# Optimization experiments

Measured on AMD Instinct MI355X. Metric: run time of the kernel, lower is better.

## Reference

```python
import jax, jax.numpy as jnp
import numpy as np

B, S, H = 2, 2048, 2048
E, I, SH = 8, 768, 5632
TOP_K = 2


def setup_inputs() -> dict:
    key = jax.random.key(0)
    ks = jax.random.split(key, 8)
    sc = lambda *shape: 1.0 / np.sqrt(shape[-2] if len(shape) > 1 else 1.0)
    return {
        "hidden_states": jax.random.normal(ks[0], (B, S, H), jnp.float32),
        "router_w": jax.random.normal(ks[1], (H, E), jnp.float32) * (1.0 / np.sqrt(H)),
        "expert_gate_up_w": jax.random.normal(ks[2], (E, H, 2 * I), jnp.float32) * (1.0 / np.sqrt(H)),
        "expert_down_w": jax.random.normal(ks[3], (E, I, H), jnp.float32) * (1.0 / np.sqrt(I)),
        "shared_gate_w": jax.random.normal(ks[4], (H, SH), jnp.float32) * (1.0 / np.sqrt(H)),
        "shared_up_w": jax.random.normal(ks[5], (H, SH), jnp.float32) * (1.0 / np.sqrt(H)),
        "shared_down_w": jax.random.normal(ks[6], (SH, H), jnp.float32) * (1.0 / np.sqrt(SH)),
        "shared_expert_gate_w": jax.random.normal(ks[7], (H, 1), jnp.float32) * (1.0 / np.sqrt(H)),
    }


def reference(hidden_states, router_w, expert_gate_up_w, expert_down_w,
              shared_gate_w, shared_up_w, shared_down_w, shared_expert_gate_w):
    b, s, h = hidden_states.shape
    x = hidden_states.reshape(-1, h)  # [T, H]

    # Shared expert (SwiGLU) gated by sigmoid scalar gate per token.
    gate = jax.nn.silu((x @ shared_gate_w).astype(jnp.float32)).astype(x.dtype)
    shared_out = (gate * (x @ shared_up_w)) @ shared_down_w  # [T, H]
    shared_out = jax.nn.sigmoid(x @ shared_expert_gate_w) * shared_out

    # Router: softmax -> top-k -> renormalize -> dense routing weights [E, T].
    router_logits = x @ router_w  # [T, E]
    router_probs = jax.nn.softmax(router_logits, axis=-1)
    top_p, top_i = jax.lax.top_k(router_probs, TOP_K)  # [T, k]
    top_p = top_p / jnp.sum(top_p, axis=-1, keepdims=True)
    one_hot = jax.nn.one_hot(top_i, E, dtype=top_p.dtype)  # [T, k, E]
    routing_full = jnp.sum(one_hot * top_p[..., None], axis=1)  # [T, E]
    routing_full = routing_full.T.astype(x.dtype)  # [E, T]

    # Dense per-expert SwiGLU over all tokens (as in source einsums).
    gate_up = jnp.einsum('th,ehm->etm', x, expert_gate_up_w)  # [E, T, 2I]
    g, u = jnp.split(gate_up, 2, axis=-1)
    g = jax.nn.silu(g.astype(jnp.float32)).astype(x.dtype)
    expert_out = jnp.einsum('eti,eih->eth', u * g, expert_down_w)  # [E, T, H]

    expert_contribution = jnp.sum(expert_out * routing_full[:, :, None], axis=0)  # [T, H]
    out = (expert_contribution + shared_out).reshape(b, s, h)
    return out, router_logits
```

## Files before the change

kernel.cpp:

```cpp
#include <hip/hip_runtime.h>
#include <hip/hip_bf16.h>
#include <stdint.h>

#define DEVFN static __device__ __forceinline__

typedef __attribute__((ext_vector_type(8))) short bf16x8;
typedef __attribute__((ext_vector_type(4))) float f32x4;
typedef unsigned short u16;
typedef unsigned int u32;
typedef unsigned long long u64;

DEVFN u16 f2bf(float f) {
    union { float f; u32 u; } v; v.f = f;
    u32 r = v.u + 0x7FFFu + ((v.u >> 16) & 1u);
    return (u16)(r >> 16);
}

DEVFN void g2l16(const void* g, void* l) {
    __builtin_amdgcn_global_load_lds(
        (const __attribute__((address_space(1))) u32*)g,
        (__attribute__((address_space(3))) u32*)l, 16, 0, 0);
}

DEVFN void hbar() {
    __asm__ __volatile__("" ::: "memory");
    __builtin_amdgcn_s_barrier();
    __asm__ __volatile__("" ::: "memory");
}
DEVFN void vm4() { asm volatile("s_waitcnt vmcnt(4)" ::: "memory"); }
DEVFN void vm0() { asm volatile("s_waitcnt vmcnt(0)" ::: "memory"); }

#define MFMA16(a, b, c) __builtin_amdgcn_mfma_f32_16x16x32_bf16(a, b, c, 0, 0, 0)

__global__ __launch_bounds__(512, 2) void gemm8_swiglu_k(
    const u16* __restrict__ A, const u16* __restrict__ Bg,
    const u16* __restrict__ Bu, u16* __restrict__ out,
    int K, int nx, int ldc)
{
    extern __shared__ char smraw[];
    char* smA = smraw;
    char* smB = smraw + 65536;

    const int tid = threadIdx.x;
    const int lane = tid & 63, wv = tid >> 6;
    const int wm = wv >> 2, wn = wv & 3;
    const int l15 = lane & 15, kg = lane >> 4;

    const int nwg = gridDim.x;
    const int id = (blockIdx.x & 7) * (nwg >> 3) + (blockIdx.x >> 3);
    const int m0 = (id / nx) * 256, n0 = (id % nx) * 128;

    const u16* Ap  = A  + (long)m0 * K;
    const u16* Bgp = Bg + (long)n0 * K;
    const u16* Bup = Bu + (long)n0 * K;

    f32x4 accg[8][2], accu[8][2];
#pragma unroll
    for (int i = 0; i < 8; ++i)
#pragma unroll
        for (int j = 0; j < 2; ++j) {
            accg[i][j] = f32x4{0.f, 0.f, 0.f, 0.f};
            accu[i][j] = f32x4{0.f, 0.f, 0.f, 0.f};
        }

    auto stA = [&](int kt, int hh, int buf) {
        const u16* src = Ap + ((long)hh * 128) * K + kt * 64;
        char* dst = smA + buf * 32768 + hh * 16384;
#pragma unroll
        for (int i = 0; i < 2; ++i) {
            int slot = i * 512 + tid;
            int row = slot >> 3, ch = slot & 7;
            g2l16(src + (long)row * K + ((ch ^ (row & 7)) << 3), dst + slot * 16);
        }
    };
    auto stB = [&](int kt, int hh, int buf) {
        const u16* src = (hh ? Bup : Bgp) + kt * 64;
        char* dst = smB + buf * 32768 + hh * 16384;
#pragma unroll
        for (int i = 0; i < 2; ++i) {
            int slot = i * 512 + tid;
            int row = slot >> 3, ch = slot & 7;
            g2l16(src + (long)row * K + ((ch ^ (row & 7)) << 3), dst + slot * 16);
        }
    };
    auto frag = [&](const char* base, int r, int c) -> bf16x8 {
        return *(const __attribute__((address_space(3))) bf16x8*)
            (base + r * 128 + (((c) ^ (r & 7)) << 4));
    };

    stA(0, 0, 0); stA(0, 1, 0);
    stB(0, 0, 0); stB(0, 1, 0);
    stB(1, 0, 1); stB(1, 1, 1);
    vm4();
    hbar();

    const int nk = K >> 6;
    for (int kt = 0; kt < nk; kt += 2) {
        const bool more = (kt + 2) < nk;
#pragma unroll
        for (int h = 0; h < 2; ++h) {
            const char* ab = smA + h * 32768;
            const char* bb = smB + h * 32768;
            bf16x8 bgv[2][2], buv[2][2];
#pragma unroll
            for (int p = 0; p < 4; ++p) {
                if (p == 0) {
#pragma unroll
                    for (int fn = 0; fn < 2; ++fn)
#pragma unroll
                        for (int s = 0; s < 2; ++s) {
                            int rB = wn * 32 + fn * 16 + l15;
                            bgv[fn][s] = frag(bb, rB, s * 4 + kg);
                            buv[fn][s] = frag(bb + 16384, rB, s * 4 + kg);
                        }
                }
                bf16x8 av[2][2];
#pragma unroll
                for (int am = 0; am < 2; ++am)
#pragma unroll
                    for (int s = 0; s < 2; ++s)
                        av[am][s] = frag(ab, wm * 128 + (p * 2 + am) * 16 + l15,
                                         s * 4 + kg);
                if (h == 0) {
                    if (p == 1)      { stA(kt + 1, 0, 1); stA(kt + 1, 1, 1); }
                    else if (p == 2) { if (more) stB(kt + 2, 0, 0); }
                    else if (p == 3) {
                        if (more) { stB(kt + 2, 1, 0); vm4(); } else vm0();
                    }
                } else {
                    if (more) {
                        if (p == 1)      stA(kt + 2, 0, 0);
                        else if (p == 2) { stA(kt + 2, 1, 0); stB(kt + 3, 0, 1); }
                        else if (p == 3) { stB(kt + 3, 1, 1); vm4(); }
                    }
                }
                hbar();
                __builtin_amdgcn_sched_barrier(0);
                __builtin_amdgcn_s_setprio(1);
#pragma unroll
                for (int am = 0; am < 2; ++am)
#pragma unroll
                    for (int s = 0; s < 2; ++s)
#pragma unroll
                        for (int fn = 0; fn < 2; ++fn) {
                            accg[p * 2 + am][fn] = MFMA16(av[am][s], bgv[fn][s],
                                                          accg[p * 2 + am][fn]);
                            accu[p * 2 + am][fn] = MFMA16(av[am][s], buv[fn][s],
                                                          accu[p * 2 + am][fn]);
                        }
                __builtin_amdgcn_s_setprio(0);
            }
        }
    }

    const int lq = lane >> 4;
#pragma unroll
    for (int fm = 0; fm < 8; ++fm)
#pragma unroll
        for (int j = 0; j < 4; ++j) {
            int row = m0 + wm * 128 + fm * 16 + lq * 4 + j;
#pragma unroll
            for (int fn = 0; fn < 2; ++fn) {
                int col = n0 + wn * 32 + fn * 16 + l15;
                float g = accg[fm][fn][j], u = accu[fm][fn][j];
                float s = g * (1.f / (1.f + __expf(-g))) * u;
                out[(long)row * ldc + col] = f2bf(s);
            }
        }
}

__global__ __launch_bounds__(512, 2) void gemm8e_swiglu_k(
    const u16* __restrict__ xb, const u16* __restrict__ Beg,
    const u16* __restrict__ Beu, const int* __restrict__ tok,
    const int* __restrict__ cntp, u16* __restrict__ eact,
    int K, int ldc, int cap)
{
    const int e = blockIdx.z;
    const int m0 = blockIdx.y * 256;
    if (m0 >= cntp[e]) return;
    const int n0 = blockIdx.x * 128;

    extern __shared__ char smraw[];
    char* smA = smraw;
    char* smB = smraw + 65536;

    const int tid = threadIdx.x;
    const int lane = tid & 63, wv = tid >> 6;
    const int wm = wv >> 2, wn = wv & 3;
    const int l15 = lane & 15, kg = lane >> 4;

    const int r0 = tid >> 3, ch = tid & 7;
    const int swz = (ch ^ (r0 & 7)) << 3;
    const int* tseg = tok + (long)e * cap + m0;
    const u16* pa00 = xb + (long)tseg[r0] * K + swz;
    const u16* pa01 = xb + (long)tseg[64 + r0] * K + swz;
    const u16* pa10 = xb + (long)tseg[128 + r0] * K + swz;
    const u16* pa11 = xb + (long)tseg[192 + r0] * K + swz;

    const u16* Bgp = Beg + ((long)e * ldc + n0) * K;
    const u16* Bup = Beu + ((long)e * ldc + n0) * K;

    f32x4 accg[8][2], accu[8][2];
#pragma unroll
    for (int i = 0; i < 8; ++i)
#pragma unroll
        for (int j = 0; j < 2; ++j) {
            accg[i][j] = f32x4{0.f, 0.f, 0.f, 0.f};
            accu[i][j] = f32x4{0.f, 0.f, 0.f, 0.f};
        }

    auto stA = [&](int kt, int hh, int buf) {
        char* dst = smA + buf * 32768 + hh * 16384;
        const u16* p0 = hh ? pa10 : pa00;
        const u16* p1 = hh ? pa11 : pa01;
        g2l16(p0 + kt * 64, dst + (long)tid * 16);
        g2l16(p1 + kt * 64, dst + (long)(512 + tid) * 16);
    };
    auto stB = [&](int kt, int hh, int buf) {
        const u16* src = (hh ? Bup : Bgp) + kt * 64;
        char* dst = smB + buf * 32768 + hh * 16384;
#pragma unroll
        for (int i = 0; i < 2; ++i) {
            int slot = i * 512 + tid;
            int row = slot >> 3, c = slot & 7;
            g2l16(src + (long)row * K + ((c ^ (row & 7)) << 3), dst + slot * 16);
        }
    };
    auto frag = [&](const char* base, int r, int c) -> bf16x8 {
        return *(const __attribute__((address_space(3))) bf16x8*)
            (base + r * 128 + (((c) ^ (r & 7)) << 4));
    };

    stA(0, 0, 0); stA(0, 1, 0);
    stB(0, 0, 0); stB(0, 1, 0);
    stB(1, 0, 1); stB(1, 1, 1);
    vm4();
    hbar();

    const int nk = K >> 6;
    for (int kt = 0; kt < nk; kt += 2) {
        const bool more = (kt + 2) < nk;
#pragma unroll
        for (int h = 0; h < 2; ++h) {
            const char* ab = smA + h * 32768;
            const char* bb = smB + h * 32768;
            bf16x8 bgv[2][2], buv[2][2];
#pragma unroll
            for (int p = 0; p < 4; ++p) {
                if (p == 0) {
#pragma unroll
                    for (int fn = 0; fn < 2; ++fn)
#pragma unroll
                        for (int s = 0; s < 2; ++s) {
                            int rB = wn * 32 + fn * 16 + l15;
                            bgv[fn][s] = frag(bb, rB, s * 4 + kg);
                            buv[fn][s] = frag(bb + 16384, rB, s * 4 + kg);
                        }
                }
                bf16x8 av[2][2];
#pragma unroll
                for (int am = 0; am < 2; ++am)
#pragma unroll
                    for (int s = 0; s < 2; ++s)
                        av[am][s] = frag(ab, wm * 128 + (p * 2 + am) * 16 + l15,
                                         s * 4 + kg);
                if (h == 0) {
                    if (p == 0)      { stA(kt + 1, 0, 1); stA(kt + 1, 1, 1); }
                    else if (p == 1) { if (more) stB(kt + 2, 0, 0); }
                    else if (p == 2) { if (more) stB(kt + 2, 1, 0); }
                    else             { if (more) vm4(); else vm0(); }
                } else {
                    if (more) {
                        if (p == 0)      stA(kt + 2, 0, 0);
                        else if (p == 1) stA(kt + 2, 1, 0);
                        else if (p == 2) stB(kt + 3, 0, 1);
                        else             { stB(kt + 3, 1, 1); vm4(); }
                    }
                }
                hbar();
                __builtin_amdgcn_sched_barrier(0);
                __builtin_amdgcn_s_setprio(1);
#pragma unroll
                for (int am = 0; am < 2; ++am)
#pragma unroll
                    for (int s = 0; s < 2; ++s)
#pragma unroll
                        for (int fn = 0; fn < 2; ++fn) {
                            accg[p * 2 + am][fn] = MFMA16(av[am][s], bgv[fn][s],
                                                          accg[p * 2 + am][fn]);
                            accu[p * 2 + am][fn] = MFMA16(av[am][s], buv[fn][s],
                                                          accu[p * 2 + am][fn]);
                        }
                __builtin_amdgcn_s_setprio(0);
                __builtin_amdgcn_sched_barrier(0);
                hbar();
            }
        }
    }

    const int lq = lane >> 4;
#pragma unroll
    for (int fm = 0; fm < 8; ++fm)
#pragma unroll
        for (int j = 0; j < 4; ++j) {
            long row = (long)e * cap + m0 + wm * 128 + fm * 16 + lq * 4 + j;
#pragma unroll
            for (int fn = 0; fn < 2; ++fn) {
                int col = n0 + wn * 32 + fn * 16 + l15;
                float g = accg[fm][fn][j], u = accu[fm][fn][j];
                float s = g * (1.f / (1.f + __expf(-g))) * u;
                eact[row * ldc + col] = f2bf(s);
            }
        }
}

template<int NSLOT>
DEVFN void stage(const u16* __restrict__ src, int ldk, u16* lds, int tid) {
#pragma unroll
    for (int i = 0; i < NSLOT / 256; ++i) {
        int slot = i * 256 + tid;
        int row = slot >> 2, chunk = slot & 3;
        int kg = chunk ^ ((row >> 1) & 3);
        g2l16(src + (long)row * ldk + kg * 8, lds + slot * 8);
    }
}

DEVFN bf16x8 ld_frag(const u16* lds, int row, int kg) {
    int chunk = kg ^ ((row >> 1) & 3);
    const u16* p = lds + row * 32 + chunk * 8;
    return *(const __attribute__((address_space(3))) bf16x8*)p;
}

__global__ __launch_bounds__(256) void gemm_down_k(
    const u16* __restrict__ A, const u16* __restrict__ B,
    float* __restrict__ C, const float* __restrict__ gvec,
    int K, int ldc)
{
    __shared__ u16 sm[2][8192];
    const int tid = threadIdx.x;
    const int lane = tid & 63, wv = tid >> 6;
    const int wm = wv >> 1, wn = wv & 1;
    const int m0 = blockIdx.y * 128, n0 = blockIdx.x * 128;
    const u16* Ab = A + (long)m0 * K;
    const u16* Bb = B + (long)n0 * K;

    f32x4 acc[4][4];
#pragma unroll
    for (int i = 0; i < 4; ++i)
#pragma unroll
        for (int j = 0; j < 4; ++j) acc[i][j] = f32x4{0.f, 0.f, 0.f, 0.f};

    stage<512>(Ab, K, &sm[0][0], tid);
    stage<512>(Bb, K, &sm[0][4096], tid);

    const int nk = K >> 5;
    for (int kt = 0; kt < nk; ++kt) {
        const int cur = kt & 1;
        __syncthreads();
        if (kt + 1 < nk) {
            stage<512>(Ab + (kt + 1) * 32, K, &sm[cur ^ 1][0], tid);
            stage<512>(Bb + (kt + 1) * 32, K, &sm[cur ^ 1][4096], tid);
        }
        const int l15 = lane & 15, kg = lane >> 4;
        bf16x8 av[4], bv[4];
#pragma unroll
        for (int f = 0; f < 4; ++f) {
            av[f] = ld_frag(&sm[cur][0],    wm * 64 + f * 16 + l15, kg);
            bv[f] = ld_frag(&sm[cur][4096], wn * 64 + f * 16 + l15, kg);
        }
#pragma unroll
        for (int fm = 0; fm < 4; ++fm)
#pragma unroll
            for (int fn = 0; fn < 4; ++fn)
                acc[fm][fn] = MFMA16(av[fm], bv[fn], acc[fm][fn]);
    }

    const int l15 = lane & 15, lq = lane >> 4;
#pragma unroll
    for (int fm = 0; fm < 4; ++fm) {
#pragma unroll
        for (int j = 0; j < 4; ++j) {
            int row = m0 + wm * 64 + fm * 16 + lq * 4 + j;
            float gmul = gvec[row];
#pragma unroll
            for (int fn = 0; fn < 4; ++fn) {
                int col = n0 + wn * 64 + fn * 16 + l15;
                C[(long)row * ldc + col] = acc[fm][fn][j] * gmul;
            }
        }
    }
}

__global__ __launch_bounds__(256) void gemm_down_moe_k(
    const u16* __restrict__ eact, const u16* __restrict__ Bed,
    float* __restrict__ out, const int* __restrict__ tok,
    const float* __restrict__ wrow, const int* __restrict__ cntp,
    int K, int ldc, int cap)
{
    const int e = blockIdx.z;
    const int m0 = blockIdx.y * 128;
    if (m0 >= cntp[e]) return;
    const int n0 = blockIdx.x * 128;

    __shared__ u16 sm[2][8192];
    const int tid = threadIdx.x;
    const int lane = tid & 63, wv = tid >> 6;
    const int wm = wv >> 1, wn = wv & 1;
    const u16* Ab = eact + ((long)e * cap + m0) * K;
    const u16* Bb = Bed + (long)e * ldc * K + (long)n0 * K;

    f32x4 acc[4][4];
#pragma unroll
    for (int i = 0; i < 4; ++i)
#pragma unroll
        for (int j = 0; j < 4; ++j) acc[i][j] = f32x4{0.f, 0.f, 0.f, 0.f};

    stage<512>(Ab, K, &sm[0][0], tid);
    stage<512>(Bb, K, &sm[0][4096], tid);

    const int nk = K >> 5;
    for (int kt = 0; kt < nk; ++kt) {
        const int cur = kt & 1;
        __syncthreads();
        if (kt + 1 < nk) {
            stage<512>(Ab + (kt + 1) * 32, K, &sm[cur ^ 1][0], tid);
            stage<512>(Bb + (kt + 1) * 32, K, &sm[cur ^ 1][4096], tid);
        }
        const int l15 = lane & 15, kg = lane >> 4;
        bf16x8 av[4], bv[4];
#pragma unroll
        for (int f = 0; f < 4; ++f) {
            av[f] = ld_frag(&sm[cur][0],    wm * 64 + f * 16 + l15, kg);
            bv[f] = ld_frag(&sm[cur][4096], wn * 64 + f * 16 + l15, kg);
        }
#pragma unroll
        for (int fm = 0; fm < 4; ++fm)
#pragma unroll
            for (int fn = 0; fn < 4; ++fn)
                acc[fm][fn] = MFMA16(av[fm], bv[fn], acc[fm][fn]);
    }

    const int l15 = lane & 15, lq = lane >> 4;
#pragma unroll
    for (int fm = 0; fm < 4; ++fm) {
#pragma unroll
        for (int j = 0; j < 4; ++j) {
            long crow = (long)e * cap + m0 + wm * 64 + fm * 16 + lq * 4 + j;
            float w = wrow[crow];
            if (w != 0.f) {
                long t = tok[crow];
#pragma unroll
                for (int fn = 0; fn < 4; ++fn) {
                    int col = n0 + wn * 64 + fn * 16 + l15;
                    atomicAdd(out + t * ldc + col, acc[fm][fn][j] * w);
                }
            }
        }
    }
}

__global__ __launch_bounds__(256) void router_k(
    const float* __restrict__ x, const float* __restrict__ rw,
    const float* __restrict__ sgw, float* __restrict__ logits,
    int2* __restrict__ te, float2* __restrict__ tw,
    float* __restrict__ sig, int T, int H)
{
    const int tid = threadIdx.x, lane = tid & 63, wv = tid >> 6;
    const int t = blockIdx.x * 4 + wv;
    const float* xr = x + (long)t * H;
    float acc[8] = {0, 0, 0, 0, 0, 0, 0, 0};
    float as = 0.f;
    for (int h = lane; h < H; h += 64) {
        float xv = xr[h];
        const float* r = rw + h * 8;
#pragma unroll
        for (int e = 0; e < 8; ++e) acc[e] += xv * r[e];
        as += xv * sgw[h];
    }
#pragma unroll
    for (int off = 32; off; off >>= 1) {
#pragma unroll
        for (int e = 0; e < 8; ++e) acc[e] += __shfl_xor(acc[e], off);
        as += __shfl_xor(as, off);
    }
    if (lane == 0) {
        float mx = acc[0];
#pragma unroll
        for (int e = 1; e < 8; ++e) mx = fmaxf(mx, acc[e]);
        float p[8], sum = 0.f;
#pragma unroll
        for (int e = 0; e < 8; ++e) { p[e] = expf(acc[e] - mx); sum += p[e]; }
        int i1 = 0;
#pragma unroll
        for (int e = 1; e < 8; ++e) if (p[e] > p[i1]) i1 = e;
        int i2 = (i1 == 0) ? 1 : 0;
#pragma unroll
        for (int e = 0; e < 8; ++e) if (e != i1 && p[e] > p[i2]) i2 = e;
        float den = p[i1] + p[i2];
        te[t] = make_int2(i1, i2);
        tw[t] = make_float2(p[i1] / den, p[i2] / den);
#pragma unroll
        for (int e = 0; e < 8; ++e) logits[(long)t * 8 + e] = acc[e];
        sig[t] = 1.f / (1.f + expf(-as));
    }
}

__global__ __launch_bounds__(256) void compact_k(
    const int2* __restrict__ te, const float2* __restrict__ tw,
    int* __restrict__ tok, float* __restrict__ wrow,
    int* __restrict__ cntp, int T, int cap)
{
    const int e = blockIdx.x;
    const int tid = threadIdx.x, lane = tid & 63, wv = tid >> 6;
    __shared__ int wtot[4];
    int cnt = 0;
    for (int c0 = 0; c0 < T; c0 += 256) {
        int t = c0 + tid;
        int2 ids = te[t];
        float2 ws = tw[t];
        float w = (ids.x == e) ? ws.x : ((ids.y == e) ? ws.y : -1.f);
        bool sel = (w >= 0.f);
        u64 b = __ballot(sel);
        int rln = __popcll(b & ((1ull << lane) - 1ull));
        if (lane == 0) wtot[wv] = __popcll(b);
        __syncthreads();
        int rank = rln, tot = 0;
#pragma unroll
        for (int k = 0; k < 4; ++k) { if (k < wv) rank += wtot[k]; tot += wtot[k]; }
        if (sel) {
            int pos = cnt + rank;
            if (pos < cap) {
                tok[(long)e * cap + pos] = t;
                wrow[(long)e * cap + pos] = w;
            }
        }
        cnt += tot;
        __syncthreads();
    }
    if (cnt > cap) cnt = cap;
    int cp = (cnt + 255) & ~255;
    if (cp > cap) cp = cap;
    for (int p = cnt + tid; p < cp; p += 256) {
        tok[(long)e * cap + p] = 0;
        wrow[(long)e * cap + p] = 0.f;
    }
    if (tid == 0) cntp[e] = cp;
}

__global__ __launch_bounds__(256) void transpose_k(
    const float* __restrict__ src0, long src_zstr, int src_ld,
    u16* __restrict__ dst0, long dst_zstr, int dst_ld)
{
    __shared__ float tile[64][65];
    const float* src = src0 + (long)blockIdx.z * src_zstr;
    u16* dst = dst0 + (long)blockIdx.z * dst_zstr;
    int r0 = blockIdx.y * 64, c0 = blockIdx.x * 64;
    int tx = threadIdx.x & 63, ty = threadIdx.x >> 6;
#pragma unroll
    for (int k = 0; k < 16; ++k)
        tile[ty + 4 * k][tx] = src[(long)(r0 + ty + 4 * k) * src_ld + c0 + tx];
    __syncthreads();
#pragma unroll
    for (int k = 0; k < 16; ++k)
        dst[(long)(c0 + ty + 4 * k) * dst_ld + r0 + tx] = f2bf(tile[tx][ty + 4 * k]);
}

__global__ __launch_bounds__(256) void cvt_x_k(const float* __restrict__ x,
                                               u16* __restrict__ xb)
{
    long i = ((long)blockIdx.x * 256 + threadIdx.x) * 4;
    float4 v = *(const float4*)(x + i);
    union { u16 s[4]; uint2 v2; } o;
    o.s[0] = f2bf(v.x); o.s[1] = f2bf(v.y); o.s[2] = f2bf(v.z); o.s[3] = f2bf(v.w);
    *(uint2*)(xb + i) = o.v2;
}

extern "C" void kernel_launch(void* const* d_in, const int* in_sizes, int n_in,
                              void* d_out, int out_size, void* d_ws, size_t ws_size,
                              hipStream_t stream) {
    (void)in_sizes; (void)n_in; (void)out_size; (void)ws_size;
    const int Hd = 2048, E = 8, I = 768, SH = 5632, T = 4096, CAP = 2048;

    const float* x    = (const float*)d_in[0];
    const float* rw   = (const float*)d_in[1];
    const float* egu  = (const float*)d_in[2];
    const float* edw  = (const float*)d_in[3];
    const float* sgw  = (const float*)d_in[4];
    const float* suw  = (const float*)d_in[5];
    const float* sdw  = (const float*)d_in[6];
    const float* segw = (const float*)d_in[7];
    float* out = (float*)d_out;
    float* logits = out + (size_t)T * Hd;

    char* wsp = (char*)d_ws;
    size_t off = 0;
    auto alloc = [&](size_t bytes) {
        void* p = wsp + off; off += (bytes + 255) & ~(size_t)255; return p;
    };
    u16* xb   = (u16*)alloc((size_t)T * Hd * 2);
    u16* Bgs  = (u16*)alloc((size_t)SH * Hd * 2);
    u16* Bus  = (u16*)alloc((size_t)SH * Hd * 2);
    u16* Bds  = (u16*)alloc((size_t)Hd * SH * 2);
    u16* Beg  = (u16*)alloc((size_t)E * I * Hd * 2);
    u16* Beu  = (u16*)alloc((size_t)E * I * Hd * 2);
    u16* Bed  = (u16*)alloc((size_t)E * Hd * I * 2);
    u16* hs   = (u16*)alloc((size_t)T * SH * 2);
    u16* eact = (u16*)alloc((size_t)E * CAP * I * 2);
    int2*   te   = (int2*)alloc((size_t)T * 8);
    float2* tw   = (float2*)alloc((size_t)T * 8);
    int*    tok  = (int*)alloc((size_t)E * CAP * 4);
    float*  wrow = (float*)alloc((size_t)E * CAP * 4);
    int*    cntp = (int*)alloc(64);
    float*  sig  = (float*)alloc((size_t)T * 4);

    hipFuncSetAttribute((const void*)gemm8_swiglu_k,
                        hipFuncAttributeMaxDynamicSharedMemorySize, 131072);
    hipFuncSetAttribute((const void*)gemm8e_swiglu_k,
                        hipFuncAttributeMaxDynamicSharedMemorySize, 131072);

    cvt_x_k<<<(T * Hd) / 1024, 256, 0, stream>>>(x, xb);
    router_k<<<T / 4, 256, 0, stream>>>(x, rw, segw, logits, te, tw, sig, T, Hd);
    compact_k<<<E, 256, 0, stream>>>(te, tw, tok, wrow, cntp, T, CAP);

    transpose_k<<<dim3(SH / 64, Hd / 64), 256, 0, stream>>>(sgw, 0, SH, Bgs, 0, Hd);
    transpose_k<<<dim3(SH / 64, Hd / 64), 256, 0, stream>>>(suw, 0, SH, Bus, 0, Hd);
    transpose_k<<<dim3(Hd / 64, SH / 64), 256, 0, stream>>>(sdw, 0, Hd, Bds, 0, SH);
    transpose_k<<<dim3(I / 64, Hd / 64, E), 256, 0, stream>>>(
        egu, (long)Hd * 2 * I, 2 * I, Beg, (long)I * Hd, Hd);
    transpose_k<<<dim3(I / 64, Hd / 64, E), 256, 0, stream>>>(
        egu + I, (long)Hd * 2 * I, 2 * I, Beu, (long)I * Hd, Hd);
    transpose_k<<<dim3(Hd / 64, I / 64, E), 256, 0, stream>>>(
        edw, (long)I * Hd, Hd, Bed, (long)Hd * I, I);

    gemm8_swiglu_k<<<dim3((SH / 128) * (T / 256)), 512, 131072, stream>>>(
        xb, Bgs, Bus, hs, Hd, SH / 128, SH);
    gemm_down_k<<<dim3(Hd / 128, T / 128), 256, 0, stream>>>(
        hs, Bds, out, sig, SH, Hd);
    gemm8e_swiglu_k<<<dim3(I / 128, CAP / 256, E), 512, 131072, stream>>>(
        xb, Beg, Beu, tok, cntp, eact, Hd, I, CAP);
    gemm_down_moe_k<<<dim3(Hd / 128, CAP / 128, E), 256, 0, stream>>>(
        eact, Bed, out, tok, wrow, cntp, I, Hd, CAP);
}
```

Before: 581.3 us.

## Fuse shared and routed expert GEMMs into single grouped launches

Merges the shared-expert and routed-expert gate/up SwiGLU GEMMs into one kernel launch with a block-index split, and likewise merges both down-projection GEMMs into one launch. Shared-expert down output now accumulates via atomicAdd into a zeroed output buffer, allowing both paths to run concurrently and fill the GPU better. This removes launch gaps and tail underutilization, at the cost of extra atomics and a memset on the shared path.

After: 582.7 us. Within noise of the previous version (+0.2%).

```diff
diff --git a/kernel.cpp b/kernel.cpp
--- a/kernel.cpp
+++ b/kernel.cpp
@@ -32,10 +32,14 @@
 
 #define MFMA16(a, b, c) __builtin_amdgcn_mfma_f32_16x16x32_bf16(a, b, c, 0, 0, 0)
 
-__global__ __launch_bounds__(512, 2) void gemm8_swiglu_k(
-    const u16* __restrict__ A, const u16* __restrict__ Bg,
-    const u16* __restrict__ Bu, u16* __restrict__ out,
-    int K, int nx, int ldc)
+__global__ __launch_bounds__(512, 2) void gemm8_top_k(
+    const u16* __restrict__ xb,
+    const u16* __restrict__ Bgs, const u16* __restrict__ Bus,
+    u16* __restrict__ hs,
+    const u16* __restrict__ Beg, const u16* __restrict__ Beu,
+    const int* __restrict__ tok, const int* __restrict__ cntp,
+    u16* __restrict__ eact,
+    int K, int nwsw, int nxsw, int ldsw, int Ie, int cap)
 {
     extern __shared__ char smraw[];
     char* smA = smraw;
@@ -45,273 +49,260 @@
     const int lane = tid & 63, wv = tid >> 6;
     const int wm = wv >> 2, wn = wv & 3;
     const int l15 = lane & 15, kg = lane >> 4;
-
-    const int nwg = gridDim.x;
-    const int id = (blockIdx.x & 7) * (nwg >> 3) + (blockIdx.x >> 3);
-    const int m0 = (id / nx) * 256, n0 = (id % nx) * 128;
-
-    const u16* Ap  = A  + (long)m0 * K;
-    const u16* Bgp = Bg + (long)n0 * K;
-    const u16* Bup = Bu + (long)n0 * K;
-
-    f32x4 accg[8][2], accu[8][2];
-#pragma unroll
-    for (int i = 0; i < 8; ++i)
-#pragma unroll
-        for (int j = 0; j < 2; ++j) {
-            accg[i][j] = f32x4{0.f, 0.f, 0.f, 0.f};
-            accu[i][j] = f32x4{0.f, 0.f, 0.f, 0.f};
-        }
-
-    auto stA = [&](int kt, int hh, int buf) {
-        const u16* src = Ap + ((long)hh * 128) * K + kt * 64;
-        char* dst = smA + buf * 32768 + hh * 16384;
-#pragma unroll
-        for (int i = 0; i < 2; ++i) {
-            int slot = i * 512 + tid;
-            int row = slot >> 3, ch = slot & 7;
-            g2l16(src + (long)row * K + ((ch ^ (row & 7)) << 3), dst + slot * 16);
-        }
-    };
-    auto stB = [&](int kt, int hh, int buf) {
-        const u16* src = (hh ? Bup : Bgp) + kt * 64;
-        char* dst = smB + buf * 32768 + hh * 16384;
-#pragma unroll
-        for (int i = 0; i < 2; ++i) {
-            int slot = i * 512 + tid;
-            int row = slot >> 3, ch = slot & 7;
-            g2l16(src + (long)row * K + ((ch ^ (row & 7)) << 3), dst + slot * 16);
-        }
-    };
+    const int lq = lane >> 4;
+
     auto frag = [&](const char* base, int r, int c) -> bf16x8 {
         return *(const __attribute__((address_space(3))) bf16x8*)
             (base + r * 128 + (((c) ^ (r & 7)) << 4));
     };
 
-    stA(0, 0, 0); stA(0, 1, 0);
-    stB(0, 0, 0); stB(0, 1, 0);
-    stB(1, 0, 1); stB(1, 1, 1);
-    vm4();
-    hbar();
-
-    const int nk = K >> 6;
-    for (int kt = 0; kt < nk; kt += 2) {
-        const bool more = (kt + 2) < nk;
-#pragma unroll
-        for (int h = 0; h < 2; ++h) {
-            const char* ab = smA + h * 32768;
-            const char* bb = smB + h * 32768;
-            bf16x8 bgv[2][2], buv[2][2];
-#pragma unroll
-            for (int p = 0; p < 4; ++p) {
-                if (p == 0) {
-#pragma unroll
-                    for (int fn = 0; fn < 2; ++fn)
-#pragma unroll
-                        for (int s = 0; s < 2; ++s) {
-                            int rB = wn * 32 + fn * 16 + l15;
-                            bgv[fn][s] = frag(bb, rB, s * 4 + kg);
-                            buv[fn][s] = frag(bb + 16384, rB, s * 4 + kg);
+    if ((int)blockIdx.x < nwsw) {
+        const int id = (blockIdx.x & 7) * (nwsw >> 3) + (blockIdx.x >> 3);
+        const int m0 = (id / nxsw) * 256, n0 = (id % nxsw) * 128;
+
+        const u16* Ap  = xb  + (long)m0 * K;
+        const u16* Bgp = Bgs + (long)n0 * K;
+        const u16* Bup = Bus + (long)n0 * K;
+
+        f32x4 accg[8][2], accu[8][2];
+#pragma unroll
+        for (int i = 0; i < 8; ++i)
+#pragma unroll
+            for (int j = 0; j < 2; ++j) {
+                accg[i][j] = f32x4{0.f, 0.f, 0.f, 0.f};
+                accu[i][j] = f32x4{0.f, 0.f, 0.f, 0.f};
+            }
+
+        auto stA = [&](int kt, int hh, int buf) {
+            const u16* src = Ap + ((long)hh * 128) * K + kt * 64;
+            char* dst = smA + buf * 32768 + hh * 16384;
+#pragma unroll
+            for (int i = 0; i < 2; ++i) {
+                int slot = i * 512 + tid;
+                int row = slot >> 3, ch = slot & 7;
+                g2l16(src + (long)row * K + ((ch ^ (row & 7)) << 3),
+                      dst + slot * 16);
+            }
+        };
+        auto stB = [&](int kt, int hh, int buf) {
+            const u16* src = (hh ? Bup : Bgp) + kt * 64;
+            char* dst = smB + buf * 32768 + hh * 16384;
+#pragma unroll
+            for (int i = 0; i < 2; ++i) {
+                int slot = i * 512 + tid;
+                int row = slot >> 3, ch = slot & 7;
+                g2l16(src + (long)row * K + ((ch ^ (row & 7)) << 3),
+                      dst + slot * 16);
+            }
+        };
+
+        stA(0, 0, 0); stA(0, 1, 0);
+        stB(0, 0, 0); stB(0, 1, 0);
+        stB(1, 0, 1); stB(1, 1, 1);
+        vm4();
+        hbar();
+
+        const int nk = K >> 6;
+        for (int kt = 0; kt < nk; kt += 2) {
+            const bool more = (kt + 2) < nk;
+#pragma unroll
+            for (int h = 0; h < 2; ++h) {
+                const char* ab = smA + h * 32768;
+                const char* bb = smB + h * 32768;
+                bf16x8 bgv[2][2], buv[2][2];
+#pragma unroll
+                for (int p = 0; p < 4; ++p) {
+                    if (p == 0) {
+#pragma unroll
+                        for (int fn = 0; fn < 2; ++fn)
+#pragma unroll
+                            for (int s = 0; s < 2; ++s) {
+                                int rB = wn * 32 + fn * 16 + l15;
+                                bgv[fn][s] = frag(bb, rB, s * 4 + kg);
+                                buv[fn][s] = frag(bb + 16384, rB, s * 4 + kg);
+                            }
+                    }
+                    bf16x8 av[2][2];
+#pragma unroll
+                    for (int am = 0; am < 2; ++am)
+#pragma unroll
+                        for (int s = 0; s < 2; ++s)
+                            av[am][s] = frag(ab,
+                                wm * 128 + (p * 2 + am) * 16 + l15, s * 4 + kg);
+                    if (h == 0) {
+                        if (p == 1)      { stA(kt + 1, 0, 1); stA(kt + 1, 1, 1); }
+                        else if (p == 2) { if (more) stB(kt + 2, 0, 0); }
+                        else if (p == 3) {
+                            if (more) { stB(kt + 2, 1, 0); vm4(); } else vm0();
                         }
+                    } else {
+                        if (more) {
+                            if (p == 1)      stA(kt + 2, 0, 0);
+                            else if (p == 2) { stA(kt + 2, 1, 0);
+                                               stB(kt + 3, 0, 1); }
+                            else if (p == 3) { stB(kt + 3, 1, 1); vm4(); }
+                        }
+                    }
+                    hbar();
+                    __builtin_amdgcn_sched_barrier(0);
+                    __builtin_amdgcn_s_setprio(1);
+#pragma unroll
+                    for (int am = 0; am < 2; ++am)
+#pragma unroll
+                        for (int s = 0; s < 2; ++s)
+#pragma unroll
+                            for (int fn = 0; fn < 2; ++fn) {
+                                accg[p * 2 + am][fn] = MFMA16(av[am][s],
+                                    bgv[fn][s], accg[p * 2 + am][fn]);
+                                accu[p * 2 + am][fn] = MFMA16(av[am][s],
+                                    buv[fn][s], accu[p * 2 + am][fn]);
+                            }
+                    __builtin_amdgcn_s_setprio(0);
                 }
-                bf16x8 av[2][2];
-#pragma unroll
-                for (int am = 0; am < 2; ++am)
-#pragma unroll
-                    for (int s = 0; s < 2; ++s)
-                        av[am][s] = frag(ab, wm * 128 + (p * 2 + am) * 16 + l15,
-                                         s * 4 + kg);
-                if (h == 0) {
-                    if (p == 1)      { stA(kt + 1, 0, 1); stA(kt + 1, 1, 1); }
-                    else if (p == 2) { if (more) stB(kt + 2, 0, 0); }
-                    else if (p == 3) {
-                        if (more) { stB(kt + 2, 1, 0); vm4(); } else vm0();
+            }
+        }
+
+#pragma unroll
+        for (int fm = 0; fm < 8; ++fm)
+#pragma unroll
+            for (int j = 0; j < 4; ++j) {
+                int row = m0 + wm * 128 + fm * 16 + lq * 4 + j;
+#pragma unroll
+                for (int fn = 0; fn < 2; ++fn) {
+                    int col = n0 + wn * 32 + fn * 16 + l15;
+                    float g = accg[fm][fn][j], u = accu[fm][fn][j];
+                    float s = g * (1.f / (1.f + __expf(-g))) * u;
+                    hs[(long)row * ldsw + col] = f2bf(s);
+                }
+            }
+    } else {
+        const int bx = blockIdx.x - nwsw;
+        const int e = bx / 48;
+        const int rem = bx % 48;
+        const int m0 = (rem / 6) * 256;
+        if (m0 >= cntp[e]) return;
+        const int n0 = (rem % 6) * 128;
+
+        const int r0 = tid >> 3, ch = tid & 7;
+        const int swz = (ch ^ (r0 & 7)) << 3;
+        const int* tseg = tok + (long)e * cap + m0;
+        const u16* pa00 = xb + (long)tseg[r0] * K + swz;
+        const u16* pa01 = xb + (long)tseg[64 + r0] * K + swz;
+        const u16* pa10 = xb + (long)tseg[128 + r0] * K + swz;
+        const u16* pa11 = xb + (long)tseg[192 + r0] * K + swz;
+
+        const u16* Bgp = Beg + ((long)e * Ie + n0) * K;
+        const u16* Bup = Beu + ((long)e * Ie + n0) * K;
+
+        f32x4 accg[8][2], accu[8][2];
+#pragma unroll
+        for (int i = 0; i < 8; ++i)
+#pragma unroll
+            for (int j = 0; j < 2; ++j) {
+                accg[i][j] = f32x4{0.f, 0.f, 0.f, 0.f};
+                accu[i][j] = f32x4{0.f, 0.f, 0.f, 0.f};
+            }
+
+        auto stA = [&](int kt, int hh, int buf) {
+            char* dst = smA + buf * 32768 + hh * 16384;
+            const u16* p0 = hh ? pa10 : pa00;
+            const u16* p1 = hh ? pa11 : pa01;
+            g2l16(p0 + kt * 64, dst + (long)tid * 16);
+            g2l16(p1 + kt * 64, dst + (long)(512 + tid) * 16);
+        };
+        auto stB = [&](int kt, int hh, int buf) {
+            const u16* src = (hh ? Bup : Bgp) + kt * 64;
+            char* dst = smB + buf * 32768 + hh * 16384;
+#pragma unroll
+            for (int i = 0; i < 2; ++i) {
+                int slot = i * 512 + tid;
+                int row = slot >> 3, c = slot & 7;
+                g2l16(src + (long)row * K + ((c ^ (row & 7)) << 3),
+                      dst + slot * 16);
+            }
+        };
+
+        stA(0, 0, 0); stA(0, 1, 0);
+        stB(0, 0, 0); stB(0, 1, 0);
+        stB(1, 0, 1); stB(1, 1, 1);
+        vm4();
+        hbar();
+
+        const int nk = K >> 6;
+        for (int kt = 0; kt < nk; kt += 2) {
+            const bool more = (kt + 2) < nk;
+#pragma unroll
+            for (int h = 0; h < 2; ++h) {
+                const char* ab = smA + h * 32768;
+                const char* bb = smB + h * 32768;
+                bf16x8 bgv[2][2], buv[2][2];
+#pragma unroll
+                for (int p = 0; p < 4; ++p) {
+                    if (p == 0) {
+#pragma unroll
+                        for (int fn = 0; fn < 2; ++fn)
+#pragma unroll
+                            for (int s = 0; s < 2; ++s) {
+                                int rB = wn * 32 + fn * 16 + l15;
+                                bgv[fn][s] = frag(bb, rB, s * 4 + kg);
+                                buv[fn][s] = frag(bb + 16384, rB, s * 4 + kg);
+                            }
                     }
-                } else {
-                    if (more) {
-                        if (p == 1)      stA(kt + 2, 0, 0);
-                        else if (p == 2) { stA(kt + 2, 1, 0); stB(kt + 3, 0, 1); }
-                        else if (p == 3) { stB(kt + 3, 1, 1); vm4(); }
+                    bf16x8 av[2][2];
+#pragma unroll
+                    for (int am = 0; am < 2; ++am)
+#pragma unroll
+                        for (int s = 0; s < 2; ++s)
+                            av[am][s] = frag(ab,
+                                wm * 128 + (p * 2 + am) * 16 + l15, s * 4 + kg);
+                    if (h == 0) {
+                        if (p == 0)      { stA(kt + 1, 0, 1); stA(kt + 1, 1, 1); }
+                        else if (p == 1) { if (more) stB(kt + 2, 0, 0); }
+                        else if (p == 2) { if (more) stB(kt + 2, 1, 0); }
+                        else             { if (more) vm4(); else vm0(); }
+                    } else {
+                        if (more) {
+                            if (p == 0)      stA(kt + 2, 0, 0);
+                            else if (p == 1) stA(kt + 2, 1, 0);
+                            else if (p == 2) stB(kt + 3, 0, 1);
+                            else             { stB(kt + 3, 1, 1); vm4(); }
+                        }
                     }
+                    hbar();
+                    __builtin_amdgcn_sched_barrier(0);
+                    __builtin_amdgcn_s_setprio(1);
+#pragma unroll
+                    for (int am = 0; am < 2; ++am)
+#pragma unroll
+                        for (int s = 0; s < 2; ++s)
+#pragma unroll
+                            for (int fn = 0; fn < 2; ++fn) {
+                                accg[p * 2 + am][fn] = MFMA16(av[am][s],
+                                    bgv[fn][s], accg[p * 2 + am][fn]);
+                                accu[p * 2 + am][fn] = MFMA16(av[am][s],
+                                    buv[fn][s], accu[p * 2 + am][fn]);
+                            }
+                    __builtin_amdgcn_s_setprio(0);
+                    __builtin_amdgcn_sched_barrier(0);
+                    hbar();
                 }
-                hbar();
-                __builtin_amdgcn_sched_barrier(0);
-                __builtin_amdgcn_s_setprio(1);
-#pragma unroll
-                for (int am = 0; am < 2; ++am)
-#pragma unroll
-                    for (int s = 0; s < 2; ++s)
-#pragma unroll
-                        for (int fn = 0; fn < 2; ++fn) {
-                            accg[p * 2 + am][fn] = MFMA16(av[am][s], bgv[fn][s],
-                                                          accg[p * 2 + am][fn]);
-                            accu[p * 2 + am][fn] = MFMA16(av[am][s], buv[fn][s],
-                                                          accu[p * 2 + am][fn]);
-                        }
-                __builtin_amdgcn_s_setprio(0);
             }
         }
-    }
-
-    const int lq = lane >> 4;
-#pragma unroll
-    for (int fm = 0; fm < 8; ++fm)
-#pragma unroll
-        for (int j = 0; j < 4; ++j) {
-            int row = m0 + wm * 128 + fm * 16 + lq * 4 + j;
-#pragma unroll
-            for (int fn = 0; fn < 2; ++fn) {
-                int col = n0 + wn * 32 + fn * 16 + l15;
-                float g = accg[fm][fn][j], u = accu[fm][fn][j];
-                float s = g * (1.f / (1.f + __expf(-g))) * u;
-                out[(long)row * ldc + col] = f2bf(s);
-            }
-        }
-}
-
-__global__ __launch_bounds__(512, 2) void gemm8e_swiglu_k(
-    const u16* __restrict__ xb, const u16* __restrict__ Beg,
-    const u16* __restrict__ Beu, const int* __restrict__ tok,
-    const int* __restrict__ cntp, u16* __restrict__ eact,
-    int K, int ldc, int cap)
-{
-    const int e = blockIdx.z;
-    const int m0 = blockIdx.y * 256;
-    if (m0 >= cntp[e]) return;
-    const int n0 = blockIdx.x * 128;
-
-    extern __shared__ char smraw[];
-    char* smA = smraw;
-    char* smB = smraw + 65536;
-
-    const int tid = threadIdx.x;
-    const int lane = tid & 63, wv = tid >> 6;
-    const int wm = wv >> 2, wn = wv & 3;
-    const int l15 = lane & 15, kg = lane >> 4;
-
-    const int r0 = tid >> 3, ch = tid & 7;
-    const int swz = (ch ^ (r0 & 7)) << 3;
-    const int* tseg = tok + (long)e * cap + m0;
-    const u16* pa00 = xb + (long)tseg[r0] * K + swz;
-    const u16* pa01 = xb + (long)tseg[64 + r0] * K + swz;
-    const u16* pa10 = xb + (long)tseg[128 + r0] * K + swz;
-    const u16* pa11 = xb + (long)tseg[192 + r0] * K + swz;
-
-    const u16* Bgp = Beg + ((long)e * ldc + n0) * K;
-    const u16* Bup = Beu + ((long)e * ldc + n0) * K;
-
-    f32x4 accg[8][2], accu[8][2];
-#pragma unroll
-    for (int i = 0; i < 8; ++i)
-#pragma unroll
-        for (int j = 0; j < 2; ++j) {
-            accg[i][j] = f32x4{0.f, 0.f, 0.f, 0.f};
-            accu[i][j] = f32x4{0.f, 0.f, 0.f, 0.f};
-        }
-
-    auto stA = [&](int kt, int hh, int buf) {
-        char* dst = smA + buf * 32768 + hh * 16384;
-        const u16* p0 = hh ? pa10 : pa00;
-        const u16* p1 = hh ? pa11 : pa01;
-        g2l16(p0 + kt * 64, dst + (long)tid * 16);
-        g2l16(p1 + kt * 64, dst + (long)(512 + tid) * 16);
-    };
-    auto stB = [&](int kt, int hh, int buf) {
-        const u16* src = (hh ? Bup : Bgp) + kt * 64;
-        char* dst = smB + buf * 32768 + hh * 16384;
-#pragma unroll
-        for (int i = 0; i < 2; ++i) {
-            int slot = i * 512 + tid;
-            int row = slot >> 3, c = slot & 7;
-            g2l16(src + (long)row * K + ((c ^ (row & 7)) << 3), dst + slot * 16);
-        }
-    };
-    auto frag = [&](const char* base, int r, int c) -> bf16x8 {
-        return *(const __attribute__((address_space(3))) bf16x8*)
-            (base + r * 128 + (((c) ^ (r & 7)) << 4));
-    };
-
-    stA(0, 0, 0); stA(0, 1, 0);
-    stB(0, 0, 0); stB(0, 1, 0);
-    stB(1, 0, 1); stB(1, 1, 1);
-    vm4();
-    hbar();
-
-    const int nk = K >> 6;
-    for (int kt = 0; kt < nk; kt += 2) {
-        const bool more = (kt + 2) < nk;
-#pragma unroll
-        for (int h = 0; h < 2; ++h) {
-            const char* ab = smA + h * 32768;
-            const char* bb = smB + h * 32768;
-            bf16x8 bgv[2][2], buv[2][2];
-#pragma unroll
-            for (int p = 0; p < 4; ++p) {
-                if (p == 0) {
-#pragma unroll
-                    for (int fn = 0; fn < 2; ++fn)
-#pragma unroll
-                        for (int s = 0; s < 2; ++s) {
-                            int rB = wn * 32 + fn * 16 + l15;
-                            bgv[fn][s] = frag(bb, rB, s * 4 + kg);
-                            buv[fn][s] = frag(bb + 16384, rB, s * 4 + kg);
-                        }
+
+#pragma unroll
+        for (int fm = 0; fm < 8; ++fm)
+#pragma unroll
+            for (int j = 0; j < 4; ++j) {
+                long row = (long)e * cap + m0 + wm * 128 + fm * 16 + lq * 4 + j;
+#pragma unroll
+                for (int fn = 0; fn < 2; ++fn) {
+                    int col = n0 + wn * 32 + fn * 16 + l15;
+                    float g = accg[fm][fn][j], u = accu[fm][fn][j];
+                    float s = g * (1.f / (1.f + __expf(-g))) * u;
+                    eact[row * Ie + col] = f2bf(s);
                 }
-                bf16x8 av[2][2];
-#pragma unroll
-                for (int am = 0; am < 2; ++am)
-#pragma unroll
-                    for (int s = 0; s < 2; ++s)
-                        av[am][s] = frag(ab, wm * 128 + (p * 2 + am) * 16 + l15,
-                                         s * 4 + kg);
-                if (h == 0) {
-                    if (p == 0)      { stA(kt + 1, 0, 1); stA(kt + 1, 1, 1); }
-                    else if (p == 1) { if (more) stB(kt + 2, 0, 0); }
-                    else if (p == 2) { if (more) stB(kt + 2, 1, 0); }
-                    else             { if (more) vm4(); else vm0(); }
-                } else {
-                    if (more) {
-                        if (p == 0)      stA(kt + 2, 0, 0);
-                        else if (p == 1) stA(kt + 2, 1, 0);
-                        else if (p == 2) stB(kt + 3, 0, 1);
-                        else             { stB(kt + 3, 1, 1); vm4(); }
-                    }
-                }
-                hbar();
-                __builtin_amdgcn_sched_barrier(0);
-                __builtin_amdgcn_s_setprio(1);
-#pragma unroll
-                for (int am = 0; am < 2; ++am)
-#pragma unroll
-                    for (int s = 0; s < 2; ++s)
-#pragma unroll
-                        for (int fn = 0; fn < 2; ++fn) {
-                            accg[p * 2 + am][fn] = MFMA16(av[am][s], bgv[fn][s],
-                                                          accg[p * 2 + am][fn]);
-                            accu[p * 2 + am][fn] = MFMA16(av[am][s], buv[fn][s],
-                                                          accu[p * 2 + am][fn]);
-                        }
-                __builtin_amdgcn_s_setprio(0);
-                __builtin_amdgcn_sched_barrier(0);
-                hbar();
-            }
-        }
-    }
-
-    const int lq = lane >> 4;
-#pragma unroll
-    for (int fm = 0; fm < 8; ++fm)
-#pragma unroll
-        for (int j = 0; j < 4; ++j) {
-            long row = (long)e * cap + m0 + wm * 128 + fm * 16 + lq * 4 + j;
-#pragma unroll
-            for (int fn = 0; fn < 2; ++fn) {
-                int col = n0 + wn * 32 + fn * 16 + l15;
-                float g = accg[fm][fn][j], u = accu[fm][fn][j];
-                float s = g * (1.f / (1.f + __expf(-g))) * u;
-                eact[row * ldc + col] = f2bf(s);
-            }
-        }
+            }
+    }
 }
 
 template<int NSLOT>
@@ -331,18 +322,43 @@
     return *(const __attribute__((address_space(3))) bf16x8*)p;
 }
 
-__global__ __launch_bounds__(256) void gemm_down_k(
-    const u16* __restrict__ A, const u16* __restrict__ B,
-    float* __restrict__ C, const float* __restrict__ gvec,
-    int K, int ldc)
+__global__ __launch_bounds__(256) void gemm_down_fused_k(
+    const u16* __restrict__ hs, const u16* __restrict__ Bds,
+    const float* __restrict__ sig,
+    const u16* __restrict__ eact, const u16* __restrict__ Bed,
+    const int* __restrict__ tok, const float* __restrict__ wrow,
+    const int* __restrict__ cntp,
+    float* __restrict__ out,
+    int Ksh, int Ke, int ldc, int cap, int nwsd)
 {
     __shared__ u16 sm[2][8192];
     const int tid = threadIdx.x;
     const int lane = tid & 63, wv = tid >> 6;
     const int wm = wv >> 1, wn = wv & 1;
-    const int m0 = blockIdx.y * 128, n0 = blockIdx.x * 128;
-    const u16* Ab = A + (long)m0 * K;
-    const u16* Bb = B + (long)n0 * K;
+    const int l15 = lane & 15, kg = lane >> 4, lq = lane >> 4;
+
+    const u16 *Ab, *Bb;
+    int K;
+    int m0, n0;
+    int e = 0;
+    bool shared_path = ((int)blockIdx.x < nwsd);
+    if (shared_path) {
+        m0 = (blockIdx.x / 16) * 128;
+        n0 = (blockIdx.x % 16) * 128;
+        K = Ksh;
+        Ab = hs + (long)m0 * K;
+        Bb = Bds + (long)n0 * K;
+    } else {
+        int bx = blockIdx.x - nwsd;
+        e = bx >> 8;
+        int rem = bx & 255;
+        m0 = (rem >> 4) * 128;
+        if (m0 >= cntp[e]) return;
+        n0 = (rem & 15) * 128;
+        K = Ke;
+        Ab = eact + ((long)e * cap + m0) * K;
+        Bb = Bed + ((long)e * ldc + n0) * K;
+    }
 
     f32x4 acc[4][4];
 #pragma unroll
@@ -361,7 +377,6 @@
             stage<512>(Ab + (kt + 1) * 32, K, &sm[cur ^ 1][0], tid);
             stage<512>(Bb + (kt + 1) * 32, K, &sm[cur ^ 1][4096], tid);
         }
-        const int l15 = lane & 15, kg = lane >> 4;
         bf16x8 av[4], bv[4];
 #pragma unroll
         for (int f = 0; f < 4; ++f) {
@@ -375,87 +390,36 @@
                 acc[fm][fn] = MFMA16(av[fm], bv[fn], acc[fm][fn]);
     }
 
-    const int l15 = lane & 15, lq = lane >> 4;
-#pragma unroll
-    for (int fm = 0; fm < 4; ++fm) {
-#pragma unroll
-        for (int j = 0; j < 4; ++j) {
-            int row = m0 + wm * 64 + fm * 16 + lq * 4 + j;
-            float gmul = gvec[row];
-#pragma unroll
-            for (int fn = 0; fn < 4; ++fn) {
-                int col = n0 + wn * 64 + fn * 16 + l15;
-                C[(long)row * ldc + col] = acc[fm][fn][j] * gmul;
-            }
-        }
-    }
-}
-
-__global__ __launch_bounds__(256) void gemm_down_moe_k(
-    const u16* __restrict__ eact, const u16* __restrict__ Bed,
-    float* __restrict__ out, const int* __restrict__ tok,
-    const float* __restrict__ wrow, const int* __restrict__ cntp,
-    int K, int ldc, int cap)
-{
-    const int e = blockIdx.z;
-    const int m0 = blockIdx.y * 128;
-    if (m0 >= cntp[e]) return;
-    const int n0 = blockIdx.x * 128;
-
-    __shared__ u16 sm[2][8192];
-    const int tid = threadIdx.x;
-    const int lane = tid & 63, wv = tid >> 6;
-    const int wm = wv >> 1, wn = wv & 1;
-    const u16* Ab = eact + ((long)e * cap + m0) * K;
-    const u16* Bb = Bed + (long)e * ldc * K + (long)n0 * K;
-
-    f32x4 acc[4][4];
-#pragma unroll
-    for (int i = 0; i < 4; ++i)
-#pragma unroll
-        for (int j = 0; j < 4; ++j) acc[i][j] = f32x4{0.f, 0.f, 0.f, 0.f};
-
-    stage<512>(Ab, K, &sm[0][0], tid);
-    stage<512>(Bb, K, &sm[0][4096], tid);
-
-    const int nk = K >> 5;
-    for (int kt = 0; kt < nk; ++kt) {
-        const int cur = kt & 1;
-        __syncthreads();
-        if (kt + 1 < nk) {
-            stage<512>(Ab + (kt + 1) * 32, K, &sm[cur ^ 1][0], tid);
-            stage<512>(Bb + (kt + 1) * 32, K, &sm[cur ^ 1][4096], tid);
-        }
-        const int l15 = lane & 15, kg = lane >> 4;
-        bf16x8 av[4], bv[4];
-#pragma unroll
-        for (int f = 0; f < 4; ++f) {
-            av[f] = ld_frag(&sm[cur][0],    wm * 64 + f * 16 + l15, kg);
-            bv[f] = ld_frag(&sm[cur][4096], wn * 64 + f * 16 + l15, kg);
-        }
+    if (shared_path) {
 #pragma unroll
         for (int fm = 0; fm < 4; ++fm)
 #pragma unroll
-            for (int fn = 0; fn < 4; ++fn)
-                acc[fm][fn] = MFMA16(av[fm], bv[fn], acc[fm][fn]);
-    }
-
-    const int l15 = lane & 15, lq = lane >> 4;
-#pragma unroll
-    for (int fm = 0; fm < 4; ++fm) {
-#pragma unroll
-        for (int j = 0; j < 4; ++j) {
-            long crow = (long)e * cap + m0 + wm * 64 + fm * 16 + lq * 4 + j;
-            float w = wrow[crow];
-            if (w != 0.f) {
-                long t = tok[crow];
+            for (int j = 0; j < 4; ++j) {
+                int row = m0 + wm * 64 + fm * 16 + lq * 4 + j;
+                float gmul = sig[row];
 #pragma unroll
                 for (int fn = 0; fn < 4; ++fn) {
                     int col = n0 + wn * 64 + fn * 16 + l15;
-                    atomicAdd(out + t * ldc + col, acc[fm][fn][j] * w);
+                    atomicAdd(out + (long)row * ldc + col,
+                              acc[fm][fn][j] * gmul);
                 }
             }
-        }
+    } else {
+#pragma unroll
+        for (int fm = 0; fm < 4; ++fm)
+#pragma unroll
+            for (int j = 0; j < 4; ++j) {
+                long crow = (long)e * cap + m0 + wm * 64 + fm * 16 + lq * 4 + j;
+                float w = wrow[crow];
+                if (w != 0.f) {
+                    long t = tok[crow];
+#pragma unroll
+                    for (int fn = 0; fn < 4; ++fn) {
+                        int col = n0 + wn * 64 + fn * 16 + l15;
+                        atomicAdd(out + t * ldc + col, acc[fm][fn][j] * w);
+                    }
+                }
+            }
     }
 }
 
@@ -613,11 +577,10 @@
     int*    cntp = (int*)alloc(64);
     float*  sig  = (float*)alloc((size_t)T * 4);
 
-    hipFuncSetAttribute((const void*)gemm8_swiglu_k,
+    hipFuncSetAttribute((const void*)gemm8_top_k,
                         hipFuncAttributeMaxDynamicSharedMemorySize, 131072);
-    hipFuncSetAttribute((const void*)gemm8e_swiglu_k,
-                        hipFuncAttributeMaxDynamicSharedMemorySize, 131072);
-
+
+    hipMemsetAsync(out, 0, (size_t)T * Hd * 4, stream);
     cvt_x_k<<<(T * Hd) / 1024, 256, 0, stream>>>(x, xb);
     router_k<<<T / 4, 256, 0, stream>>>(x, rw, segw, logits, te, tw, sig, T, Hd);
     compact_k<<<E, 256, 0, stream>>>(te, tw, tok, wrow, cntp, T, CAP);
@@ -632,12 +595,12 @@
     transpose_k<<<dim3(Hd / 64, I / 64, E), 256, 0, stream>>>(
         edw, (long)I * Hd, Hd, Bed, (long)Hd * I, I);
 
-    gemm8_swiglu_k<<<dim3((SH / 128) * (T / 256)), 512, 131072, stream>>>(
-        xb, Bgs, Bus, hs, Hd, SH / 128, SH);
-    gemm_down_k<<<dim3(Hd / 128, T / 128), 256, 0, stream>>>(
-        hs, Bds, out, sig, SH, Hd);
-    gemm8e_swiglu_k<<<dim3(I / 128, CAP / 256, E), 512, 131072, stream>>>(
-        xb, Beg, Beu, tok, cntp, eact, Hd, I, CAP);
-    gemm_down_moe_k<<<dim3(Hd / 128, CAP / 128, E), 256, 0, stream>>>(
-        eact, Bed, out, tok, wrow, cntp, I, Hd, CAP);
-}
+    const int NWSW = (SH / 128) * (T / 256);
+    gemm8_top_k<<<dim3(NWSW + 6 * (CAP / 256) * E), 512, 131072, stream>>>(
+        xb, Bgs, Bus, hs, Beg, Beu, tok, cntp, eact,
+        Hd, NWSW, SH / 128, SH, I, CAP);
+    const int NWSD = (T / 128) * (Hd / 128);
+    gemm_down_fused_k<<<dim3(NWSD + 256 * E), 256, 0, stream>>>(
+        hs, Bds, sig, eact, Bed, tok, wrow, cntp, out,
+        SH, I, Hd, CAP, NWSD);
+}
```
